# Performance work log

Hardware: AMD Instinct MI355X
Metric: run time of the kernel (lower is better)

## Reference

```python
import jax, jax.numpy as jnp
import numpy as np

N_NODES = 50000
N_EDGES = 800000
H = 128            # node_hidden_size
T = 2              # num_prop_rounds


def setup_inputs() -> dict:
    key = jax.random.key(0)
    ks = jax.random.split(key, 10)
    hv = jax.random.normal(ks[0], (N_NODES, H), dtype=jnp.float32)
    he = jax.random.normal(ks[1], (N_EDGES, 1), dtype=jnp.float32)
    src = jax.random.randint(ks[2], (N_EDGES,), 0, N_NODES, dtype=jnp.int32)
    dst = jax.random.randint(ks[3], (N_EDGES,), 0, N_NODES, dtype=jnp.int32)
    # per-round params, stacked on leading T axis; small scale to avoid gate saturation
    W_msg = jax.random.normal(ks[4], (T, 2 * H, 2 * H + 1), dtype=jnp.float32) * 0.05
    b_msg = jax.random.normal(ks[5], (T, 2 * H), dtype=jnp.float32) * 0.05
    W_ih = jax.random.normal(ks[6], (T, 3 * H, 2 * H), dtype=jnp.float32) * 0.05
    W_hh = jax.random.normal(ks[7], (T, 3 * H, H), dtype=jnp.float32) * 0.05
    b_ih = jax.random.normal(ks[8], (T, 3 * H), dtype=jnp.float32) * 0.05
    b_hh = jax.random.normal(ks[9], (T, 3 * H), dtype=jnp.float32) * 0.05
    return dict(hv=hv, he=he, src=src, dst=dst, W_msg=W_msg, b_msg=b_msg,
                W_ih=W_ih, W_hh=W_hh, b_ih=b_ih, b_hh=b_hh)


def _gru_cell(x, h, W_ih, W_hh, b_ih, b_hh):
    # torch.nn.GRUCell math
    gi = x @ W_ih.T + b_ih          # [N, 3H]
    gh = h @ W_hh.T + b_hh          # [N, 3H]
    i_r, i_z, i_n = jnp.split(gi, 3, axis=1)
    h_r, h_z, h_n = jnp.split(gh, 3, axis=1)
    r = jax.nn.sigmoid(i_r + h_r)
    z = jax.nn.sigmoid(i_z + h_z)
    n = jnp.tanh(i_n + r * h_n)
    return (1.0 - z) * n + z * h


def reference(hv, he, src, dst, W_msg, b_msg, W_ih, W_hh, b_ih, b_hh):
    n_nodes = hv.shape[0]
    for t in range(T):
        # per-edge message input: concat([hv_dst, hv_src, he])  [E, 2H+1]
        msg_in = jnp.concatenate([hv[dst], hv[src], he], axis=1)
        edge_act = msg_in @ W_msg[t].T + b_msg[t]          # [E, 2H]
        # ragged sum-reduce over incoming edges (deg-0 nodes get zeros)
        a = jax.ops.segment_sum(edge_act, dst, num_segments=n_nodes)  # [N, 2H]
        hv = _gru_cell(a, hv, W_ih[t], W_hh[t], b_ih[t], b_hh[t])
    return hv
```

## Files before the change

### kernel.cpp

```cpp
#include <hip/hip_runtime.h>
#include <cstdint>
#include <cstddef>

#define N_NODES 50000
#define N_EDGES 800000
#define HDIM 128
#define TROUNDS 2
#define NTILES 3125
#define PACK_PER_T (416 * 64)
#define MAXDEG 64

typedef __attribute__((ext_vector_type(8))) _Float16 half8v;
typedef __attribute__((ext_vector_type(2))) _Float16 half2v;
typedef __attribute__((ext_vector_type(4))) float f32x4;
typedef unsigned short ushort_t;

#define GLD_LDS(gp, lp)                                                        \
  __builtin_amdgcn_global_load_lds(                                            \
      (__attribute__((address_space(1))) const void*)(gp),                     \
      (__attribute__((address_space(3))) void*)(lp), 16, 0, 0)

static __device__ __forceinline__ float sigmoidf_(float x) {
  return 1.0f / (1.0f + __expf(-x));
}
static __device__ __forceinline__ float tanhf_(float x) {
  float xc = fminf(15.0f, fmaxf(-15.0f, x));
  float a = __expf(2.0f * xc);
  return (a - 1.0f) / (a + 1.0f);
}
static __device__ __forceinline__ float f16bits2f(uint32_t hb) {
  ushort_t u = (ushort_t)hb;
  _Float16 h;
  __builtin_memcpy(&h, &u, 2);
  return (float)h;
}

__global__ void pack_all(const float* __restrict__ Wmsg, const float* __restrict__ Wih,
                         const float* __restrict__ Whh, _Float16* __restrict__ W1p,
                         _Float16* __restrict__ W2p, float* __restrict__ we) {
  int g = blockIdx.x * blockDim.x + threadIdx.x;
  if (g < TROUNDS * 256) {
    int t = g >> 8, j = g & 255;
    we[g] = Wmsg[((size_t)t * 256 + j) * 257 + 256];
  }
  if (g >= TROUNDS * PACK_PER_T) return;
  int t = g / PACK_PER_T;
  int r = g % PACK_PER_T;
  int lane = r & 63;
  int fr = r >> 6;
  const float* srcp;
  _Float16* dstp;
  if (fr < 128) {
    int jt = fr >> 3, kt = fr & 7;
    int j = jt * 16 + (lane & 15);
    int k = kt * 32 + ((lane >> 4) << 3);
    srcp = Wmsg + (size_t)t * 256 * 257 + (size_t)j * 257 + k;
    dstp = W1p + ((size_t)t * 128 + fr) * 512 + lane * 8;
  } else {
    int fr2 = fr - 128;
    int chunk = fr2 / 12, idx = fr2 % 12;
    int jt = chunk / 3, pp = chunk % 3;
    int j = pp * 128 + jt * 16 + (lane & 15);
    int k;
    if (idx < 8) {
      k = idx * 32 + ((lane >> 4) << 3);
      srcp = Wih + (size_t)t * 384 * 256 + (size_t)j * 256 + k;
    } else {
      k = (idx - 8) * 32 + ((lane >> 4) << 3);
      srcp = Whh + (size_t)t * 384 * 128 + (size_t)j * 128 + k;
    }
    dstp = W2p + ((size_t)t * 288 + fr2) * 512 + lane * 8;
  }
  #pragma unroll
  for (int e = 0; e < 8; ++e) dstp[e] = (_Float16)srcp[e];
}

__global__ void cast_hv(const float* __restrict__ hv, _Float16* __restrict__ hvh) {
  int i = blockIdx.x * blockDim.x + threadIdx.x;
  if (i >= N_NODES * HDIM / 4) return;
  float4 v = reinterpret_cast<const float4*>(hv)[i];
  half2v o0, o1;
  o0[0] = (_Float16)v.x; o0[1] = (_Float16)v.y;
  o1[0] = (_Float16)v.z; o1[1] = (_Float16)v.w;
  reinterpret_cast<half2v*>(hvh)[i * 2] = o0;
  reinterpret_cast<half2v*>(hvh)[i * 2 + 1] = o1;
}

__global__ void fill_pad(const int* __restrict__ src, const int* __restrict__ dst,
                         const float* __restrict__ he, int* __restrict__ cnt,
                         uint32_t* __restrict__ csr) {
  int e = blockIdx.x * blockDim.x + threadIdx.x;
  if (e >= N_EDGES) return;
  int d = dst[e];
  int slot = atomicAdd(&cnt[d], 1);
  if (slot < MAXDEG) {
    _Float16 hh = (_Float16)he[e];
    ushort_t hb;
    __builtin_memcpy(&hb, &hh, 2);
    uint32_t en = ((uint32_t)hb << 16) | (uint32_t)src[e];
    csr[(size_t)d * MAXDEG + slot] = en;
  }
}

__global__ void gather_h(const _Float16* __restrict__ hvh, const int* __restrict__ cnt,
                         const uint32_t* __restrict__ csr, _Float16* __restrict__ S_h,
                         float* __restrict__ hsum, float* __restrict__ deg_f, int n) {
  int wid = (int)((blockIdx.x * blockDim.x + threadIdx.x) >> 6);
  int lane = threadIdx.x & 63;
  if (wid >= n) return;
  int deg = min(cnt[wid], MAXDEG);
  uint32_t ent = (lane < deg) ? csr[(size_t)wid * MAXDEG + lane] : 0u;
  float a0 = 0.f, a1 = 0.f, hs = 0.f;
  int k = 0;
  for (; k + 3 < deg; k += 4) {
    uint32_t e0 = __shfl(ent, k), e1 = __shfl(ent, k + 1);
    uint32_t e2 = __shfl(ent, k + 2), e3 = __shfl(ent, k + 3);
    half2v v0 = *reinterpret_cast<const half2v*>(hvh + (size_t)(e0 & 0xffffu) * HDIM + lane * 2);
    half2v v1 = *reinterpret_cast<const half2v*>(hvh + (size_t)(e1 & 0xffffu) * HDIM + lane * 2);
    half2v v2 = *reinterpret_cast<const half2v*>(hvh + (size_t)(e2 & 0xffffu) * HDIM + lane * 2);
    half2v v3 = *reinterpret_cast<const half2v*>(hvh + (size_t)(e3 & 0xffffu) * HDIM + lane * 2);
    a0 += ((float)v0[0] + (float)v1[0]) + ((float)v2[0] + (float)v3[0]);
    a1 += ((float)v0[1] + (float)v1[1]) + ((float)v2[1] + (float)v3[1]);
    hs += (f16bits2f(e0 >> 16) + f16bits2f(e1 >> 16)) +
          (f16bits2f(e2 >> 16) + f16bits2f(e3 >> 16));
  }
  for (; k < deg; ++k) {
    uint32_t e0 = __shfl(ent, k);
    half2v v0 = *reinterpret_cast<const half2v*>(hvh + (size_t)(e0 & 0xffffu) * HDIM + lane * 2);
    a0 += (float)v0[0];
    a1 += (float)v0[1];
    hs += f16bits2f(e0 >> 16);
  }
  half2v o;
  o[0] = (_Float16)a0;
  o[1] = (_Float16)a1;
  *reinterpret_cast<half2v*>(S_h + (size_t)wid * HDIM + lane * 2) = o;
  if (lane == 0) hsum[wid] = hs;
  if (lane == 1) deg_f[wid] = (float)deg;
}

__global__ __launch_bounds__(512, 2) void u1_kernel(
    const float* __restrict__ hv, const _Float16* __restrict__ S_h,
    const float* __restrict__ deg_f, const float* __restrict__ hsum,
    const _Float16* __restrict__ W1p, const float* __restrict__ we,
    const float* __restrict__ bmsg, _Float16* __restrict__ a_out) {
  __shared__ _Float16 buf[2][8 * 512];
  const int tid = threadIdx.x;
  const int wv = tid >> 6, lane = tid & 63;
  const int tile0 = blockIdx.x * 16 + wv * 2;
  const int tile1 = tile0 + 1;
  const bool act0 = (tile0 < NTILES), act1 = (tile1 < NTILES);
  const int koff = (lane >> 4) * 8;
  const int m0 = (lane >> 4) * 4;

  auto stage1 = [&](int c) {
    const _Float16* g = W1p + (size_t)c * 4096 + wv * 512 + lane * 8;
    GLD_LDS(g, &buf[c & 1][wv * 512]);
  };
  stage1(0);

  half8v x0[8], x1[8];
  float degs[2][4], hss[2][4];
  #pragma unroll
  for (int tt = 0; tt < 2; ++tt) {
    const int tile = tt ? tile1 : tile0;
    const bool act = tt ? act1 : act0;
    half8v* x = tt ? x1 : x0;
    if (act) {
      int rowA = tile * 16 + (lane & 15);
      float deg = deg_f[rowA];
      const float* hrow = hv + (size_t)rowA * HDIM;
      #pragma unroll
      for (int kt = 0; kt < 4; ++kt) {
        const float* sp = hrow + kt * 32 + koff;
        #pragma unroll
        for (int e = 0; e < 8; ++e) x[kt][e] = (_Float16)(sp[e] * deg);
      }
      const _Float16* srow = S_h + (size_t)rowA * HDIM + koff;
      #pragma unroll
      for (int kt = 0; kt < 4; ++kt)
        x[4 + kt] = *reinterpret_cast<const half8v*>(srow + kt * 32);
      #pragma unroll
      for (int rr = 0; rr < 4; ++rr) {
        degs[tt][rr] = deg_f[tile * 16 + m0 + rr];
        hss[tt][rr] = hsum[tile * 16 + m0 + rr];
      }
    }
  }

  #pragma unroll 1
  for (int jt = 0; jt < 16; ++jt) {
    __syncthreads();
    if (jt < 15) stage1(jt + 1);
    const _Float16* B = &buf[jt & 1][0];
    f32x4 acc0 = {0.f, 0.f, 0.f, 0.f}, acc1 = {0.f, 0.f, 0.f, 0.f};
    #pragma unroll
    for (int kt = 0; kt < 8; ++kt) {
      half8v b = *reinterpret_cast<const half8v*>(B + (size_t)kt * 512 + lane * 8);
      acc0 = __builtin_amdgcn_mfma_f32_16x16x32_f16(x0[kt], b, acc0, 0, 0, 0);
      acc1 = __builtin_amdgcn_mfma_f32_16x16x32_f16(x1[kt], b, acc1, 0, 0, 0);
    }
    int j = jt * 16 + (lane & 15);
    float bm = bmsg[j], w = we[j];
    if (act0) {
      #pragma unroll
      for (int rr = 0; rr < 4; ++rr)
        a_out[(size_t)(tile0 * 16 + m0 + rr) * 256 + j] =
            (_Float16)(acc0[rr] + degs[0][rr] * bm + hss[0][rr] * w);
    }
    if (act1) {
      #pragma unroll
      for (int rr = 0; rr < 4; ++rr)
        a_out[(size_t)(tile1 * 16 + m0 + rr) * 256 + j] =
            (_Float16)(acc1[rr] + degs[1][rr] * bm + hss[1][rr] * w);
    }
  }
}

__global__ __launch_bounds__(512, 2) void u2_kernel(
    const float* __restrict__ hv_in, const _Float16* __restrict__ a_in,
    const _Float16* __restrict__ W2p, const float* __restrict__ bih,
    const float* __restrict__ bhh, float* __restrict__ hv_out,
    _Float16* __restrict__ hvh_out) {
  __shared__ _Float16 buf[2][12 * 512];
  const int tid = threadIdx.x;
  const int wv = tid >> 6, lane = tid & 63;
  const int tile0 = blockIdx.x * 16 + wv * 2;
  const int tile1 = tile0 + 1;
  const bool act0 = (tile0 < NTILES), act1 = (tile1 < NTILES);
  const int koff = (lane >> 4) * 8;
  const int m0 = (lane >> 4) * 4;

  auto stage = [&](int c) {
    const _Float16* g = W2p + (size_t)c * 6144 + wv * 512 + lane * 8;
    GLD_LDS(g, &buf[c & 1][wv * 512]);
    if (wv < 4) {
      const _Float16* g2 = W2p + (size_t)c * 6144 + (8 + wv) * 512 + lane * 8;
      GLD_LDS(g2, &buf[c & 1][(8 + wv) * 512]);
    }
  };
  stage(0);

  half8v a80[8], a81[8], h40[4], h41[4];
  #pragma unroll
  for (int tt = 0; tt < 2; ++tt) {
    const int tile = tt ? tile1 : tile0;
    const bool act = tt ? act1 : act0;
    half8v* a8 = tt ? a81 : a80;
    half8v* h4 = tt ? h41 : h40;
    if (act) {
      int rowA = tile * 16 + (lane & 15);
      const _Float16* ar = a_in + (size_t)rowA * 256 + koff;
      #pragma unroll
      for (int kt = 0; kt < 8; ++kt)
        a8[kt] = *reinterpret_cast<const half8v*>(ar + kt * 32);
      const float* hr = hv_in + (size_t)rowA * HDIM + koff;
      #pragma unroll
      for (int kt = 0; kt < 4; ++kt) {
        #pragma unroll
        for (int e = 0; e < 8; ++e) h4[kt][e] = (_Float16)hr[kt * 32 + e];
      }
    }
  }

  auto compute = [&](const _Float16* B, f32x4& ai0, f32x4& ag0, f32x4& ai1, f32x4& ag1) {
    ai0 = (f32x4){0.f, 0.f, 0.f, 0.f};
    ag0 = (f32x4){0.f, 0.f, 0.f, 0.f};
    ai1 = (f32x4){0.f, 0.f, 0.f, 0.f};
    ag1 = (f32x4){0.f, 0.f, 0.f, 0.f};
    #pragma unroll
    for (int kt = 0; kt < 8; ++kt) {
      half8v b = *reinterpret_cast<const half8v*>(B + (size_t)kt * 512 + lane * 8);
      ai0 = __builtin_amdgcn_mfma_f32_16x16x32_f16(a80[kt], b, ai0, 0, 0, 0);
      ai1 = __builtin_amdgcn_mfma_f32_16x16x32_f16(a81[kt], b, ai1, 0, 0, 0);
    }
    #pragma unroll
    for (int kt = 0; kt < 4; ++kt) {
      half8v b = *reinterpret_cast<const half8v*>(B + (size_t)(8 + kt) * 512 + lane * 8);
      ag0 = __builtin_amdgcn_mfma_f32_16x16x32_f16(h40[kt], b, ag0, 0, 0, 0);
      ag1 = __builtin_amdgcn_mfma_f32_16x16x32_f16(h41[kt], b, ag1, 0, 0, 0);
    }
  };

  f32x4 rreg0, rreg1, zreg0, zreg1, ai0, ag0, ai1, ag1;
  #pragma unroll 1
  for (int jt = 0; jt < 8; ++jt) {
    const int c0 = jt * 3;
    const int fcol = jt * 16 + (lane & 15);
    __syncthreads();
    stage(c0 + 1);
    compute(&buf[c0 & 1][0], ai0, ag0, ai1, ag1);
    {
      float bi = bih[fcol], bq = bhh[fcol];
      #pragma unroll
      for (int rr = 0; rr < 4; ++rr) {
        rreg0[rr] = sigmoidf_(ai0[rr] + bi + ag0[rr] + bq);
        rreg1[rr] = sigmoidf_(ai1[rr] + bi + ag1[rr] + bq);
      }
    }
    __syncthreads();
    stage(c0 + 2);
    compute(&buf[(c0 + 1) & 1][0], ai0, ag0, ai1, ag1);
    {
      float bi = bih[128 + fcol], bq = bhh[128 + fcol];
      #pragma unroll
      for (int rr = 0; rr < 4; ++rr) {
        zreg0[rr] = sigmoidf_(ai0[rr] + bi + ag0[rr] + bq);
        zreg1[rr] = sigmoidf_(ai1[rr] + bi + ag1[rr] + bq);
      }
    }
    __syncthreads();
    if (jt < 7) stage(c0 + 3);
    compute(&buf[(c0 + 2) & 1][0], ai0, ag0, ai1, ag1);
    {
      float bi = bih[256 + fcol], bq = bhh[256 + fcol];
      if (act0) {
        #pragma unroll
        for (int rr = 0; rr < 4; ++rr) {
          int node = tile0 * 16 + m0 + rr;
          float n = tanhf_(ai0[rr] + bi + rreg0[rr] * (ag0[rr] + bq));
          float h = hv_in[(size_t)node * HDIM + fcol];
          float hn = (1.f - zreg0[rr]) * n + zreg0[rr] * h;
          hv_out[(size_t)node * HDIM + fcol] = hn;
          hvh_out[(size_t)node * HDIM + fcol] = (_Float16)hn;
        }
      }
      if (act1) {
        #pragma unroll
        for (int rr = 0; rr < 4; ++rr) {
          int node = tile1 * 16 + m0 + rr;
          float n = tanhf_(ai1[rr] + bi + rreg1[rr] * (ag1[rr] + bq));
          float h = hv_in[(size_t)node * HDIM + fcol];
          float hn = (1.f - zreg1[rr]) * n + zreg1[rr] * h;
          hv_out[(size_t)node * HDIM + fcol] = hn;
          hvh_out[(size_t)node * HDIM + fcol] = (_Float16)hn;
        }
      }
    }
  }
}

extern "C" void kernel_launch(void* const* d_in, const int* in_sizes, int n_in,
                              void* d_out, int out_size, void* d_ws, size_t ws_size,
                              hipStream_t stream) {
  const float* hv   = (const float*)d_in[0];
  const float* he   = (const float*)d_in[1];
  const int*   src  = (const int*)d_in[2];
  const int*   dst  = (const int*)d_in[3];
  const float* Wmsg = (const float*)d_in[4];
  const float* bmsg = (const float*)d_in[5];
  const float* Wih  = (const float*)d_in[6];
  const float* Whh  = (const float*)d_in[7];
  const float* bih  = (const float*)d_in[8];
  const float* bhh  = (const float*)d_in[9];

  char* p = (char*)d_ws;
  auto alloc = [&](size_t bytes) { char* r = p; p += (bytes + 255) & ~(size_t)255; return r; };
  _Float16* S_h   = (_Float16*)alloc((size_t)N_NODES * HDIM * 2);
  _Float16* a_buf = (_Float16*)alloc((size_t)N_NODES * 256 * 2);
  _Float16* hvh   = (_Float16*)alloc((size_t)N_NODES * HDIM * 2);
  float*    deg_f = (float*)alloc((size_t)N_NODES * 4);
  float*    hsum  = (float*)alloc((size_t)N_NODES * 4);
  float*    we    = (float*)alloc((size_t)TROUNDS * 256 * 4);
  const size_t W1PT = (size_t)128 * 512;
  const size_t W2PT = (size_t)288 * 512;
  _Float16* W1p = (_Float16*)alloc(TROUNDS * W1PT * 2);
  _Float16* W2p = (_Float16*)alloc(TROUNDS * W2PT * 2);
  int*      cnt = (int*)alloc((size_t)N_NODES * 4);
  uint32_t* csr = (uint32_t*)alloc((size_t)N_NODES * MAXDEG * 4);

  hipMemsetAsync(cnt, 0, (size_t)N_NODES * 4, stream);

  pack_all<<<(TROUNDS * PACK_PER_T + 255) / 256, 256, 0, stream>>>(Wmsg, Wih, Whh, W1p, W2p, we);
  cast_hv<<<(N_NODES * HDIM / 4 + 255) / 256, 256, 0, stream>>>(hv, hvh);
  fill_pad<<<(N_EDGES + 255) / 256, 256, 0, stream>>>(src, dst, he, cnt, csr);

  const float* hcur = hv;
  float* outp = (float*)d_out;
  const int ugrid = (NTILES + 15) / 16;
  for (int t = 0; t < TROUNDS; ++t) {
    gather_h<<<(N_NODES + 3) / 4, 256, 0, stream>>>(hvh, cnt, csr, S_h, hsum, deg_f, N_NODES);
    u1_kernel<<<ugrid, 512, 0, stream>>>(
        hcur, S_h, deg_f, hsum, W1p + (size_t)t * W1PT,
        we + (size_t)t * 256, bmsg + (size_t)t * 256, a_buf);
    u2_kernel<<<ugrid, 512, 0, stream>>>(
        hcur, a_buf, W2p + (size_t)t * W2PT,
        bih + (size_t)t * 384, bhh + (size_t)t * 384, outp, hvh);
    hcur = outp;
  }
  (void)in_sizes; (void)n_in; (void)out_size; (void)ws_size;
}
```

Measured before the change: 255.5 us.

## Halve GEMM block size, pad degree counters, unroll gather by eight

The u1 and u2 kernels move from 512-thread blocks covering 16 tiles to 256-thread blocks covering 8 tiles, twice as many blocks, with each wave staging more weight chunks into LDS. The per-node atomic degree counters are padded to a 16-int stride so that counters for different nodes no longer share cache lines during fill_pad. The gather loop is unrolled from 4 to 8 edges to keep more independent loads in flight. Each block now loads the full weight panel for half as many rows, which raises weight traffic, and the padded counter array makes the memset 16x larger.

```diff
diff --git a/kernel.cpp b/kernel.cpp
--- a/kernel.cpp
+++ b/kernel.cpp
@@ -9,6 +9,7 @@
 #define NTILES 3125
 #define PACK_PER_T (416 * 64)
 #define MAXDEG 64
+#define CSTRIDE 16
 
 typedef __attribute__((ext_vector_type(8))) _Float16 half8v;
 typedef __attribute__((ext_vector_type(2))) _Float16 half2v;
@@ -92,7 +93,7 @@
   int e = blockIdx.x * blockDim.x + threadIdx.x;
   if (e >= N_EDGES) return;
   int d = dst[e];
-  int slot = atomicAdd(&cnt[d], 1);
+  int slot = atomicAdd(&cnt[(size_t)d * CSTRIDE], 1);
   if (slot < MAXDEG) {
     _Float16 hh = (_Float16)he[e];
     ushort_t hb;
@@ -108,21 +109,24 @@
   int wid = (int)((blockIdx.x * blockDim.x + threadIdx.x) >> 6);
   int lane = threadIdx.x & 63;
   if (wid >= n) return;
-  int deg = min(cnt[wid], MAXDEG);
+  int deg = min(cnt[(size_t)wid * CSTRIDE], MAXDEG);
   uint32_t ent = (lane < deg) ? csr[(size_t)wid * MAXDEG + lane] : 0u;
   float a0 = 0.f, a1 = 0.f, hs = 0.f;
   int k = 0;
-  for (; k + 3 < deg; k += 4) {
-    uint32_t e0 = __shfl(ent, k), e1 = __shfl(ent, k + 1);
-    uint32_t e2 = __shfl(ent, k + 2), e3 = __shfl(ent, k + 3);
-    half2v v0 = *reinterpret_cast<const half2v*>(hvh + (size_t)(e0 & 0xffffu) * HDIM + lane * 2);
-    half2v v1 = *reinterpret_cast<const half2v*>(hvh + (size_t)(e1 & 0xffffu) * HDIM + lane * 2);
-    half2v v2 = *reinterpret_cast<const half2v*>(hvh + (size_t)(e2 & 0xffffu) * HDIM + lane * 2);
-    half2v v3 = *reinterpret_cast<const half2v*>(hvh + (size_t)(e3 & 0xffffu) * HDIM + lane * 2);
-    a0 += ((float)v0[0] + (float)v1[0]) + ((float)v2[0] + (float)v3[0]);
-    a1 += ((float)v0[1] + (float)v1[1]) + ((float)v2[1] + (float)v3[1]);
-    hs += (f16bits2f(e0 >> 16) + f16bits2f(e1 >> 16)) +
-          (f16bits2f(e2 >> 16) + f16bits2f(e3 >> 16));
+  for (; k + 7 < deg; k += 8) {
+    uint32_t ee[8];
+    #pragma unroll
+    for (int q = 0; q < 8; ++q) ee[q] = __shfl(ent, k + q);
+    half2v vv[8];
+    #pragma unroll
+    for (int q = 0; q < 8; ++q)
+      vv[q] = *reinterpret_cast<const half2v*>(hvh + (size_t)(ee[q] & 0xffffu) * HDIM + lane * 2);
+    #pragma unroll
+    for (int q = 0; q < 8; ++q) {
+      a0 += (float)vv[q][0];
+      a1 += (float)vv[q][1];
+      hs += f16bits2f(ee[q] >> 16);
+    }
   }
   for (; k < deg; ++k) {
     uint32_t e0 = __shfl(ent, k);
@@ -139,7 +143,7 @@
   if (lane == 1) deg_f[wid] = (float)deg;
 }
 
-__global__ __launch_bounds__(512, 2) void u1_kernel(
+__global__ __launch_bounds__(256, 3) void u1_kernel(
     const float* __restrict__ hv, const _Float16* __restrict__ S_h,
     const float* __restrict__ deg_f, const float* __restrict__ hsum,
     const _Float16* __restrict__ W1p, const float* __restrict__ we,
@@ -147,17 +151,17 @@
   __shared__ _Float16 buf[2][8 * 512];
   const int tid = threadIdx.x;
   const int wv = tid >> 6, lane = tid & 63;
-  const int tile0 = blockIdx.x * 16 + wv * 2;
+  const int tile0 = blockIdx.x * 8 + wv * 2;
   const int tile1 = tile0 + 1;
   const bool act0 = (tile0 < NTILES), act1 = (tile1 < NTILES);
   const int koff = (lane >> 4) * 8;
   const int m0 = (lane >> 4) * 4;
 
-  auto stage1 = [&](int c) {
-    const _Float16* g = W1p + (size_t)c * 4096 + wv * 512 + lane * 8;
-    GLD_LDS(g, &buf[c & 1][wv * 512]);
-  };
-  stage1(0);
+  {
+    const _Float16* g = W1p + (size_t)(wv * 2) * 512 + lane * 8;
+    #pragma unroll
+    for (int i = 0; i < 2; ++i) GLD_LDS(g + i * 512, &buf[0][(wv * 2 + i) * 512]);
+  }
 
   half8v x0[8], x1[8];
   float degs[2][4], hss[2][4];
@@ -191,7 +195,11 @@
   #pragma unroll 1
   for (int jt = 0; jt < 16; ++jt) {
     __syncthreads();
-    if (jt < 15) stage1(jt + 1);
+    if (jt < 15) {
+      const _Float16* g = W1p + (size_t)(jt + 1) * 4096 + (size_t)(wv * 2) * 512 + lane * 8;
+      #pragma unroll
+      for (int i = 0; i < 2; ++i) GLD_LDS(g + i * 512, &buf[(jt + 1) & 1][(wv * 2 + i) * 512]);
+    }
     const _Float16* B = &buf[jt & 1][0];
     f32x4 acc0 = {0.f, 0.f, 0.f, 0.f}, acc1 = {0.f, 0.f, 0.f, 0.f};
     #pragma unroll
@@ -217,7 +225,7 @@
   }
 }
 
-__global__ __launch_bounds__(512, 2) void u2_kernel(
+__global__ __launch_bounds__(256, 2) void u2_kernel(
     const float* __restrict__ hv_in, const _Float16* __restrict__ a_in,
     const _Float16* __restrict__ W2p, const float* __restrict__ bih,
     const float* __restrict__ bhh, float* __restrict__ hv_out,
@@ -225,20 +233,19 @@
   __shared__ _Float16 buf[2][12 * 512];
   const int tid = threadIdx.x;
   const int wv = tid >> 6, lane = tid & 63;
-  const int tile0 = blockIdx.x * 16 + wv * 2;
+  const int tile0 = blockIdx.x * 8 + wv * 2;
   const int tile1 = tile0 + 1;
   const bool act0 = (tile0 < NTILES), act1 = (tile1 < NTILES);
   const int koff = (lane >> 4) * 8;
   const int m0 = (lane >> 4) * 4;
 
-  auto stage = [&](int c) {
-    const _Float16* g = W2p + (size_t)c * 6144 + wv * 512 + lane * 8;
-    GLD_LDS(g, &buf[c & 1][wv * 512]);
-    if (wv < 4) {
-      const _Float16* g2 = W2p + (size_t)c * 6144 + (8 + wv) * 512 + lane * 8;
-      GLD_LDS(g2, &buf[c & 1][(8 + wv) * 512]);
-    }
+  auto stage = [&](int n) {
+    const _Float16* g = W2p + (size_t)n * 6144 + (size_t)(wv * 3) * 512 + lane * 8;
+    _Float16* l = &buf[n & 1][(wv * 3) * 512];
+    #pragma unroll
+    for (int i = 0; i < 3; ++i) GLD_LDS(g + i * 512, l + i * 512);
   };
+
   stage(0);
 
   half8v a80[8], a81[8], h40[4], h41[4];
@@ -366,10 +373,10 @@
   const size_t W2PT = (size_t)288 * 512;
   _Float16* W1p = (_Float16*)alloc(TROUNDS * W1PT * 2);
   _Float16* W2p = (_Float16*)alloc(TROUNDS * W2PT * 2);
-  int*      cnt = (int*)alloc((size_t)N_NODES * 4);
+  int*      cnt = (int*)alloc((size_t)N_NODES * CSTRIDE * 4);
   uint32_t* csr = (uint32_t*)alloc((size_t)N_NODES * MAXDEG * 4);
 
-  hipMemsetAsync(cnt, 0, (size_t)N_NODES * 4, stream);
+  hipMemsetAsync(cnt, 0, (size_t)N_NODES * CSTRIDE * 4, stream);
 
   pack_all<<<(TROUNDS * PACK_PER_T + 255) / 256, 256, 0, stream>>>(Wmsg, Wih, Whh, W1p, W2p, we);
   cast_hv<<<(N_NODES * HDIM / 4 + 255) / 256, 256, 0, stream>>>(hv, hvh);
@@ -377,13 +384,13 @@
 
   const float* hcur = hv;
   float* outp = (float*)d_out;
-  const int ugrid = (NTILES + 15) / 16;
+  const int ugrid = (NTILES + 7) / 8;
   for (int t = 0; t < TROUNDS; ++t) {
     gather_h<<<(N_NODES + 3) / 4, 256, 0, stream>>>(hvh, cnt, csr, S_h, hsum, deg_f, N_NODES);
-    u1_kernel<<<ugrid, 512, 0, stream>>>(
+    u1_kernel<<<ugrid, 256, 0, stream>>>(
         hcur, S_h, deg_f, hsum, W1p + (size_t)t * W1PT,
         we + (size_t)t * 256, bmsg + (size_t)t * 256, a_buf);
-    u2_kernel<<<ugrid, 512, 0, stream>>>(
+    u2_kernel<<<ugrid, 256, 0, stream>>>(
         hcur, a_buf, W2p + (size_t)t * W2PT,
         bih + (size_t)t * 384, bhh + (size_t)t * 384, outp, hvh);
     hcur = outp;
```

New measurement: 253.1 us. Within noise of the previous version (-0.9%).
